# Performance work log

Hardware: AMD Instinct MI355X
Metric: run time of the kernel (lower is better)

The kernel has to match this reference:

```python
import jax, jax.numpy as jnp
import numpy as np

B, LQ, LKV, D, H, LOOKBACK = 4, 4096, 512, 512, 8, 8
DH = D // H
SCALE = DH ** -0.5


def setup_inputs() -> dict:
    key = jax.random.key(0)
    ks = jax.random.split(key, 12)
    q = jax.random.normal(ks[0], (B, LQ, D), dtype=jnp.float32)
    kv_src = jax.random.normal(ks[1], (B, LKV, D), dtype=jnp.float32)
    seg_id = jnp.sort(jax.random.randint(ks[2], (B, LQ), 0, LKV), axis=-1)
    kv_mask = jnp.zeros((B, LKV), dtype=bool)
    q_pad_mask = jnp.zeros((B, LQ), dtype=bool)
    s = D ** -0.5
    Wq = jax.random.normal(ks[3], (D, D), jnp.float32) * s
    bq = jnp.zeros((D,), jnp.float32)
    Wk = jax.random.normal(ks[4], (D, D), jnp.float32) * s
    bk = jnp.zeros((D,), jnp.float32)
    Wv = jax.random.normal(ks[5], (D, D), jnp.float32) * s
    bv = jnp.zeros((D,), jnp.float32)
    Wo = jax.random.normal(ks[6], (D, D), jnp.float32) * s
    bo = jnp.zeros((D,), jnp.float32)
    return {"q": q, "kv_src": kv_src, "seg_id": seg_id, "kv_mask": kv_mask,
            "q_pad_mask": q_pad_mask, "Wq": Wq, "bq": bq, "Wk": Wk, "bk": bk,
            "Wv": Wv, "bv": bv, "Wo": Wo, "bo": bo}


def _split_heads(x):
    b, l, _ = x.shape
    return x.reshape(b, l, H, DH).transpose(0, 2, 1, 3)  # (B,H,L,Dh)


def reference(q, kv_src, seg_id, kv_mask, q_pad_mask, Wq, bq, Wk, bk, Wv, bv, Wo, bo):
    qh = _split_heads(q @ Wq + bq)        # (B,H,Lq,Dh)
    kh = _split_heads(kv_src @ Wk + bk)   # (B,H,Lkv,Dh)
    vh = _split_heads(kv_src @ Wv + bv)   # (B,H,Lkv,Dh)

    offsets = jnp.arange(LOOKBACK + 1)
    gather = jnp.clip(seg_id[:, :, None] - offsets, 0, LKV - 1)  # (B,Lq,Kw)

    # per-batch windowed gather of K/V: (B,H,Lq,Kw,Dh)
    k_sel = jax.vmap(lambda kb, gb: kb[:, gb])(kh, gather)
    v_sel = jax.vmap(lambda vb, gb: vb[:, gb])(vh, gather)

    scores = jnp.einsum('bhld,bhlkd->bhlk', qh, k_sel) * SCALE
    mask_sel = jax.vmap(lambda m, g: m[g])(kv_mask, gather)  # (B,Lq,Kw)
    scores = jnp.where(mask_sel[:, None], jnp.finfo(scores.dtype).min, scores)
    probs = jax.nn.softmax(scores, axis=-1)

    out = jnp.einsum('bhlk,bhlkd->bhld', probs, v_sel)
    out = out.transpose(0, 2, 1, 3).reshape(q.shape[0], q.shape[1], D)
    out = out @ Wo + bo
    out = jnp.where(q_pad_mask[:, :, None], 0.0, out)
    return out
```

## Files before the change

kernel.cpp:

```cpp
#include <hip/hip_runtime.h>
#include <hip/hip_bf16.h>
#include <float.h>

typedef unsigned short u16;
typedef __attribute__((ext_vector_type(8))) short short8;
typedef __attribute__((ext_vector_type(4))) float f32x4;

#define NB       4
#define LQ       4096
#define LKV      512
#define DMODEL   512
#define NH       8
#define DH       64
#define KW       9
#define SCALE    0.125f

#define BM 64
#define BN 128
#define BK 32

__device__ inline float bf2f(u16 v) { return __uint_as_float(((unsigned)v) << 16); }
__device__ inline u16 f2bf(float f) {
    unsigned u = __float_as_uint(f);
    return (u16)((u + 0x7fffu + ((u >> 16) & 1u)) >> 16);
}
__device__ inline void gload16(const u16* g, u16* l) {
    __builtin_amdgcn_global_load_lds((const __attribute__((address_space(1))) void*)g,
                                     (__attribute__((address_space(3))) void*)l, 16, 0, 0);
}
__device__ inline short8 cvt8(const float4 v0, const float4 v1) {
    short8 s;
    s[0] = (short)f2bf(v0.x); s[1] = (short)f2bf(v0.y);
    s[2] = (short)f2bf(v0.z); s[3] = (short)f2bf(v0.w);
    s[4] = (short)f2bf(v1.x); s[5] = (short)f2bf(v1.y);
    s[6] = (short)f2bf(v1.z); s[7] = (short)f2bf(v1.w);
    return s;
}
__device__ inline int xcd_swz(int id, int nwg) {
    const int cpx = nwg >> 3;
    return (id & 7) * cpx + (id >> 3);
}

__global__ __launch_bounds__(256) void transpose4_kernel(
    const float* __restrict__ Wq, const float* __restrict__ Wk,
    const float* __restrict__ Wv, const float* __restrict__ Wo,
    u16* __restrict__ Wqt, u16* __restrict__ Wkvt, u16* __restrict__ Wot)
{
    __shared__ float tile[32][33];
    const int z = blockIdx.z;
    const float* src = (z == 0) ? Wq : (z == 1) ? Wk : (z == 2) ? Wv : Wo;
    u16* dst = (z == 0) ? Wqt : (z == 3) ? Wot : Wkvt;
    const int roff = (z == 2) ? DMODEL : 0;

    const int tx = threadIdx.x & 31, ty = threadIdx.x >> 5;
    const int x0 = blockIdx.x * 32, y0 = blockIdx.y * 32;
    #pragma unroll
    for (int i = 0; i < 4; ++i)
        tile[ty + i * 8][tx] = src[(y0 + ty + i * 8) * DMODEL + x0 + tx];
    __syncthreads();
    #pragma unroll
    for (int i = 0; i < 4; ++i)
        dst[(long long)(roff + x0 + ty + i * 8) * DMODEL + y0 + tx] = f2bf(tile[tx][ty + i * 8]);
}

template<int A_F32, int OUT_F32>
__global__ __launch_bounds__(256, 6) void gemm64_kernel(
    const void* __restrict__ Ain, const u16* __restrict__ Bt,
    const float* __restrict__ bias0, const float* __restrict__ bias1, int nsplit,
    void* __restrict__ Cout, int M, int N, int K, int cshift,
    const unsigned char* __restrict__ row_mask)
{
    __shared__ u16 As[BM * BK];
    __shared__ u16 Bs[BN * BK];

    const int tid = threadIdx.x;
    const int w = tid >> 6, l = tid & 63;
    const int wr = w >> 1, wc = w & 1;

    const int wg = xcd_swz((int)blockIdx.x, (int)gridDim.x);
    const int bx = wg & ((1 << cshift) - 1);
    const int by = wg >> cshift;
    const int brow = by * BM, bcol = bx * BN;

    const int rsub = l >> 2;
    const int csrc = (l & 3) ^ (rsub & 3);
    const u16*   gA  = (const u16*)Ain   + (long long)(brow + w * 16 + rsub) * K + csrc * 8;
    const float* gAf = (const float*)Ain + (long long)(brow + w * 16 + rsub) * K + csrc * 8;
    const u16* gB0 = Bt + (long long)(bcol + w * 32 + rsub) * K + csrc * 8;
    const u16* gB1 = gB0 + (long long)16 * K;
    u16* lA  = As + (w * 16) * BK;
    u16* lB0 = Bs + (w * 32) * BK;
    u16* lB1 = Bs + (w * 32 + 16) * BK;

    const int hi = l >> 4, lr = l & 15;
    const int cs = ((hi ^ (lr & 3)) * 8);

    f32x4 acc[2][4] = {};

    float4 v0, v1;
    if (A_F32) { v0 = *(const float4*)(gAf); v1 = *(const float4*)(gAf + 4); }

    for (int k0 = 0; k0 < K; k0 += BK) {
        if (A_F32) {
            *(short8*)(lA + l * 8) = cvt8(v0, v1);
        } else {
            gload16(gA + k0, lA);
        }
        gload16(gB0 + k0, lB0);
        gload16(gB1 + k0, lB1);
        __syncthreads();

        if (A_F32 && k0 + BK < K) {
            v0 = *(const float4*)(gAf + k0 + BK);
            v1 = *(const float4*)(gAf + k0 + BK + 4);
        }

        short8 a[2], b[4];
        #pragma unroll
        for (int m = 0; m < 2; ++m)
            a[m] = *(const short8*)&As[(wr * 32 + m * 16 + lr) * BK + cs];
        #pragma unroll
        for (int n = 0; n < 4; ++n)
            b[n] = *(const short8*)&Bs[(wc * 64 + n * 16 + lr) * BK + cs];
        #pragma unroll
        for (int m = 0; m < 2; ++m)
            #pragma unroll
            for (int n = 0; n < 4; ++n)
                acc[m][n] = __builtin_amdgcn_mfma_f32_16x16x32_bf16(a[m], b[n], acc[m][n], 0, 0, 0);
        __syncthreads();
    }

    #pragma unroll
    for (int m = 0; m < 2; ++m) {
        #pragma unroll
        for (int n = 0; n < 4; ++n) {
            const int col = bcol + wc * 64 + n * 16 + lr;
            const float bv = (col < nsplit) ? bias0[col] : bias1[col - nsplit];
            #pragma unroll
            for (int r = 0; r < 4; ++r) {
                const int row = brow + wr * 32 + m * 16 + hi * 4 + r;
                const float v = acc[m][n][r] + bv;
                if (OUT_F32) {
                    ((float*)Cout)[(long long)row * N + col] =
                        (row_mask != nullptr && row_mask[row]) ? 0.0f : v;
                } else {
                    ((u16*)Cout)[(long long)row * N + col] = f2bf(v);
                }
            }
        }
    }
}

__global__ __launch_bounds__(256, 6) void qproj_attn_kernel(
    const float* __restrict__ Aq, const u16* __restrict__ Bt,
    const float* __restrict__ bias, const u16* __restrict__ khv,
    const int* __restrict__ seg_id, const unsigned char* __restrict__ kv_mask,
    u16* __restrict__ atb)
{
    __shared__ u16 smem[BM * BN];
    u16* As = smem;
    u16* Bs = smem + BM * BK;
    u16* qt = smem;

    const int tid = threadIdx.x;
    const int w = tid >> 6, l = tid & 63;
    const int wr = w >> 1, wc = w & 1;

    const int wg = xcd_swz((int)blockIdx.x, (int)gridDim.x);
    const int bx = wg & 3;
    const int by = wg >> 2;
    const int brow = by * BM, bcol = bx * BN;
    const int K = DMODEL;

    const int rsub = l >> 2;
    const int csrc = (l & 3) ^ (rsub & 3);
    const float* gAf = Aq + (long long)(brow + w * 16 + rsub) * K + csrc * 8;
    const u16* gB0 = Bt + (long long)(bcol + w * 32 + rsub) * K + csrc * 8;
    const u16* gB1 = gB0 + (long long)16 * K;
    u16* lA  = As + (w * 16) * BK;
    u16* lB0 = Bs + (w * 32) * BK;
    u16* lB1 = Bs + (w * 32 + 16) * BK;

    const int hi = l >> 4, lr = l & 15;
    const int cs = ((hi ^ (lr & 3)) * 8);

    f32x4 acc[2][4] = {};

    float4 v0 = *(const float4*)(gAf);
    float4 v1 = *(const float4*)(gAf + 4);

    for (int k0 = 0; k0 < K; k0 += BK) {
        *(short8*)(lA + l * 8) = cvt8(v0, v1);
        gload16(gB0 + k0, lB0);
        gload16(gB1 + k0, lB1);
        __syncthreads();

        if (k0 + BK < K) {
            v0 = *(const float4*)(gAf + k0 + BK);
            v1 = *(const float4*)(gAf + k0 + BK + 4);
        }

        short8 a[2], b[4];
        #pragma unroll
        for (int m = 0; m < 2; ++m)
            a[m] = *(const short8*)&As[(wr * 32 + m * 16 + lr) * BK + cs];
        #pragma unroll
        for (int n = 0; n < 4; ++n)
            b[n] = *(const short8*)&Bs[(wc * 64 + n * 16 + lr) * BK + cs];
        #pragma unroll
        for (int m = 0; m < 2; ++m)
            #pragma unroll
            for (int n = 0; n < 4; ++n)
                acc[m][n] = __builtin_amdgcn_mfma_f32_16x16x32_bf16(a[m], b[n], acc[m][n], 0, 0, 0);
        __syncthreads();
    }

    #pragma unroll
    for (int m = 0; m < 2; ++m) {
        #pragma unroll
        for (int n = 0; n < 4; ++n) {
            const int col = wc * 64 + n * 16 + lr;
            const float bv = bias[bcol + col];
            const int g = col >> 3;
            #pragma unroll
            for (int r = 0; r < 4; ++r) {
                const int row = wr * 32 + m * 16 + hi * 4 + r;
                qt[row * BN + ((g ^ (row & 7)) << 3) + (col & 7)] =
                    f2bf(acc[m][n][r] + bv);
            }
        }
    }
    __syncthreads();

    const int dchunk = tid & 7;
    #pragma unroll
    for (int p = 0; p < 4; ++p) {
        const int it = p * 32 + (tid >> 3);
        const int row = it >> 1;
        const int h2  = it & 1;
        const long long bl = brow + row;
        const int b = (int)(bl >> 12);
        const int head = (bcol >> 6) + h2;
        const int seg = seg_id[bl];
        const unsigned char* km = kv_mask + b * LKV;
        const u16* kvb = khv + (long long)b * LKV * 1024;

        const int g = h2 * 8 + dchunk;
        const short8 q8 = *(const short8*)&qt[row * BN + ((g ^ (row & 7)) << 3)];
        float qf[8];
        #pragma unroll
        for (int e = 0; e < 8; ++e) qf[e] = bf2f((u16)q8[e]);

        int idxs[KW];
        float sc[KW];
        #pragma unroll
        for (int j = 0; j < KW; ++j) {
            int idx = seg - j;
            idx = idx < 0 ? 0 : (idx > LKV - 1 ? LKV - 1 : idx);
            idxs[j] = idx;
            const short8 k8 = *(const short8*)&kvb[(long long)idx * 1024 + head * DH + dchunk * 8];
            float d = 0.0f;
            #pragma unroll
            for (int e = 0; e < 8; ++e)
                d = fmaf(qf[e], bf2f((u16)k8[e]), d);
            d += __shfl_xor(d, 1);
            d += __shfl_xor(d, 2);
            d += __shfl_xor(d, 4);
            float s = d * SCALE;
            if (km[idx]) s = -FLT_MAX;
            sc[j] = s;
        }

        float mx = sc[0];
        #pragma unroll
        for (int j = 1; j < KW; ++j) mx = fmaxf(mx, sc[j]);
        float den = 0.0f;
        #pragma unroll
        for (int j = 0; j < KW; ++j) { sc[j] = __expf(sc[j] - mx); den += sc[j]; }
        const float inv = 1.0f / den;

        float o[8];
        #pragma unroll
        for (int e = 0; e < 8; ++e) o[e] = 0.0f;
        #pragma unroll
        for (int j = 0; j < KW; ++j) {
            const short8 v8 = *(const short8*)&kvb[(long long)idxs[j] * 1024 + DMODEL + head * DH + dchunk * 8];
            const float pj = sc[j];
            #pragma unroll
            for (int e = 0; e < 8; ++e)
                o[e] = fmaf(pj, bf2f((u16)v8[e]), o[e]);
        }

        short8 ov;
        #pragma unroll
        for (int e = 0; e < 8; ++e) ov[e] = (short)f2bf(o[e] * inv);
        *(short8*)&atb[bl * DMODEL + head * DH + dchunk * 8] = ov;
    }
}

extern "C" void kernel_launch(void* const* d_in, const int* in_sizes, int n_in,
                              void* d_out, int out_size, void* d_ws, size_t ws_size,
                              hipStream_t stream) {
    const float*         q          = (const float*)d_in[0];
    const float*         kv_src     = (const float*)d_in[1];
    const int*           seg_id     = (const int*)d_in[2];
    const unsigned char* kv_mask    = (const unsigned char*)d_in[3];
    const unsigned char* q_pad_mask = (const unsigned char*)d_in[4];
    const float*         Wq         = (const float*)d_in[5];
    const float*         bq         = (const float*)d_in[6];
    const float*         Wk         = (const float*)d_in[7];
    const float*         bk         = (const float*)d_in[8];
    const float*         Wv         = (const float*)d_in[9];
    const float*         bv         = (const float*)d_in[10];
    const float*         Wo         = (const float*)d_in[11];
    const float*         bo         = (const float*)d_in[12];
    float* out = (float*)d_out;

    const long long MQ  = (long long)NB * LQ;
    const long long MKV = (long long)NB * LKV;

    char* wsb = (char*)d_ws;
    u16* Wqt  = (u16*)wsb;  wsb += DMODEL * DMODEL * 2;
    u16* Wkvt = (u16*)wsb;  wsb += 2 * DMODEL * DMODEL * 2;
    u16* Wot  = (u16*)wsb;  wsb += DMODEL * DMODEL * 2;
    u16* khv  = (u16*)wsb;  wsb += MKV * 2 * DMODEL * 2;
    u16* atb  = (u16*)wsb;  wsb += MQ  * DMODEL * 2;

    dim3 blk(256);

    transpose4_kernel<<<dim3(DMODEL / 32, DMODEL / 32, 4), blk, 0, stream>>>(
        Wq, Wk, Wv, Wo, Wqt, Wkvt, Wot);

    gemm64_kernel<1, 0><<<dim3((unsigned)((2 * DMODEL / BN) * (MKV / BM))), blk, 0, stream>>>(
        kv_src, Wkvt, bk, bv, DMODEL, khv, (int)MKV, 2 * DMODEL, DMODEL, 3, nullptr);

    qproj_attn_kernel<<<dim3((unsigned)((DMODEL / BN) * (MQ / BM))), blk, 0, stream>>>(
        q, Wqt, bq, khv, seg_id, kv_mask, atb);

    gemm64_kernel<0, 1><<<dim3((unsigned)((DMODEL / BN) * (MQ / BM))), blk, 0, stream>>>(
        atb, Wot, bo, bo, DMODEL, out, (int)MQ, DMODEL, DMODEL, 2, q_pad_mask);
}
```

Measured before the change: 83.09 us.

## Retile GEMMs to 64x64x64 with one head per attention block

Changes the GEMM tile from 64x128 (BK 32) to 64x64 (BK 64), with an 8-chunk XOR swizzle for LDS and two MFMA k-steps per tile. It raises launch-bounds occupancy from 6 to 8 and doubles the grid. In the fused Q-projection/attention kernel each block now covers one head, so the attention phase handles 64 rows with 2 iterations instead of 4. The intent is more parallelism and fewer barrier rounds per K step, at the cost of less B-tile reuse per block and more redundant A-tile loads.

```diff
diff --git a/kernel.cpp b/kernel.cpp
--- a/kernel.cpp
+++ b/kernel.cpp
@@ -16,8 +16,8 @@
 #define SCALE    0.125f
 
 #define BM 64
-#define BN 128
-#define BK 32
+#define BN 64
+#define BK 64
 
 __device__ inline float bf2f(u16 v) { return __uint_as_float(((unsigned)v) << 16); }
 __device__ inline u16 f2bf(float f) {
@@ -64,10 +64,10 @@
 }
 
 template<int A_F32, int OUT_F32>
-__global__ __launch_bounds__(256, 6) void gemm64_kernel(
+__global__ __launch_bounds__(256, 8) void gemm64_kernel(
     const void* __restrict__ Ain, const u16* __restrict__ Bt,
     const float* __restrict__ bias0, const float* __restrict__ bias1, int nsplit,
-    void* __restrict__ Cout, int M, int N, int K, int cshift,
+    void* __restrict__ Cout, int N, int K, int cshift,
     const unsigned char* __restrict__ row_mask)
 {
     __shared__ u16 As[BM * BK];
@@ -82,59 +82,73 @@
     const int by = wg >> cshift;
     const int brow = by * BM, bcol = bx * BN;
 
-    const int rsub = l >> 2;
-    const int csrc = (l & 3) ^ (rsub & 3);
-    const u16*   gA  = (const u16*)Ain   + (long long)(brow + w * 16 + rsub) * K + csrc * 8;
-    const float* gAf = (const float*)Ain + (long long)(brow + w * 16 + rsub) * K + csrc * 8;
-    const u16* gB0 = Bt + (long long)(bcol + w * 32 + rsub) * K + csrc * 8;
-    const u16* gB1 = gB0 + (long long)16 * K;
-    u16* lA  = As + (w * 16) * BK;
-    u16* lB0 = Bs + (w * 32) * BK;
-    u16* lB1 = Bs + (w * 32 + 16) * BK;
+    const int srow   = l >> 3;
+    const int schunk = ((l & 7) ^ srow) * 8;
+    const long long ar0 = brow + w * 16 + srow;
+    const long long br0 = bcol + w * 16 + srow;
+    const u16*   gA0  = (const u16*)Ain   + ar0 * K + schunk;
+    const u16*   gA1  = gA0 + 8 * K;
+    const float* gAf0 = (const float*)Ain + ar0 * K + schunk;
+    const float* gAf1 = gAf0 + 8 * K;
+    const u16* gB0 = Bt + br0 * K + schunk;
+    const u16* gB1 = gB0 + 8 * K;
+    u16* lA0 = As + (w * 16) * BK;
+    u16* lA1 = As + (w * 16 + 8) * BK;
+    u16* lB0 = Bs + (w * 16) * BK;
+    u16* lB1 = Bs + (w * 16 + 8) * BK;
 
     const int hi = l >> 4, lr = l & 15;
-    const int cs = ((hi ^ (lr & 3)) * 8);
-
-    f32x4 acc[2][4] = {};
-
-    float4 v0, v1;
-    if (A_F32) { v0 = *(const float4*)(gAf); v1 = *(const float4*)(gAf + 4); }
+    const int r7 = lr & 7;
+
+    f32x4 acc[2][2] = {};
+
+    float4 p0, p1, p2, p3;
+    if (A_F32) {
+        p0 = *(const float4*)(gAf0);     p1 = *(const float4*)(gAf0 + 4);
+        p2 = *(const float4*)(gAf1);     p3 = *(const float4*)(gAf1 + 4);
+    }
 
     for (int k0 = 0; k0 < K; k0 += BK) {
         if (A_F32) {
-            *(short8*)(lA + l * 8) = cvt8(v0, v1);
+            *(short8*)(lA0 + l * 8) = cvt8(p0, p1);
+            *(short8*)(lA1 + l * 8) = cvt8(p2, p3);
         } else {
-            gload16(gA + k0, lA);
+            gload16(gA0 + k0, lA0);
+            gload16(gA1 + k0, lA1);
         }
         gload16(gB0 + k0, lB0);
         gload16(gB1 + k0, lB1);
         __syncthreads();
 
         if (A_F32 && k0 + BK < K) {
-            v0 = *(const float4*)(gAf + k0 + BK);
-            v1 = *(const float4*)(gAf + k0 + BK + 4);
-        }
-
-        short8 a[2], b[4];
-        #pragma unroll
-        for (int m = 0; m < 2; ++m)
-            a[m] = *(const short8*)&As[(wr * 32 + m * 16 + lr) * BK + cs];
-        #pragma unroll
-        for (int n = 0; n < 4; ++n)
-            b[n] = *(const short8*)&Bs[(wc * 64 + n * 16 + lr) * BK + cs];
-        #pragma unroll
-        for (int m = 0; m < 2; ++m)
-            #pragma unroll
-            for (int n = 0; n < 4; ++n)
-                acc[m][n] = __builtin_amdgcn_mfma_f32_16x16x32_bf16(a[m], b[n], acc[m][n], 0, 0, 0);
+            p0 = *(const float4*)(gAf0 + k0 + BK); p1 = *(const float4*)(gAf0 + k0 + BK + 4);
+            p2 = *(const float4*)(gAf1 + k0 + BK); p3 = *(const float4*)(gAf1 + k0 + BK + 4);
+        }
+
+        #pragma unroll
+        for (int g2 = 0; g2 < 2; ++g2) {
+            const int slot = ((g2 * 4 + hi) ^ r7) * 8;
+            short8 a[2], b[2];
+            #pragma unroll
+            for (int m = 0; m < 2; ++m)
+                a[m] = *(const short8*)&As[(wr * 32 + m * 16 + lr) * BK + slot];
+            #pragma unroll
+            for (int n = 0; n < 2; ++n)
+                b[n] = *(const short8*)&Bs[(wc * 32 + n * 16 + lr) * BK + slot];
+            #pragma unroll
+            for (int m = 0; m < 2; ++m)
+                #pragma unroll
+                for (int n = 0; n < 2; ++n)
+                    acc[m][n] = __builtin_amdgcn_mfma_f32_16x16x32_bf16(a[m], b[n], acc[m][n], 0, 0, 0);
+        }
         __syncthreads();
     }
 
     #pragma unroll
     for (int m = 0; m < 2; ++m) {
         #pragma unroll
-        for (int n = 0; n < 4; ++n) {
-            const int col = bcol + wc * 64 + n * 16 + lr;
+        for (int n = 0; n < 2; ++n) {
+            const int col = bcol + wc * 32 + n * 16 + lr;
             const float bv = (col < nsplit) ? bias0[col] : bias1[col - nsplit];
             #pragma unroll
             for (int r = 0; r < 4; ++r) {
@@ -151,13 +165,13 @@
     }
 }
 
-__global__ __launch_bounds__(256, 6) void qproj_attn_kernel(
+__global__ __launch_bounds__(256, 8) void qproj_attn_kernel(
     const float* __restrict__ Aq, const u16* __restrict__ Bt,
     const float* __restrict__ bias, const u16* __restrict__ khv,
     const int* __restrict__ seg_id, const unsigned char* __restrict__ kv_mask,
     u16* __restrict__ atb)
 {
-    __shared__ u16 smem[BM * BN];
+    __shared__ u16 smem[BM * BK + BN * BK];
     u16* As = smem;
     u16* Bs = smem + BM * BK;
     u16* qt = smem;
@@ -167,65 +181,73 @@
     const int wr = w >> 1, wc = w & 1;
 
     const int wg = xcd_swz((int)blockIdx.x, (int)gridDim.x);
-    const int bx = wg & 3;
-    const int by = wg >> 2;
+    const int bx = wg & 7;
+    const int by = wg >> 3;
     const int brow = by * BM, bcol = bx * BN;
     const int K = DMODEL;
 
-    const int rsub = l >> 2;
-    const int csrc = (l & 3) ^ (rsub & 3);
-    const float* gAf = Aq + (long long)(brow + w * 16 + rsub) * K + csrc * 8;
-    const u16* gB0 = Bt + (long long)(bcol + w * 32 + rsub) * K + csrc * 8;
-    const u16* gB1 = gB0 + (long long)16 * K;
-    u16* lA  = As + (w * 16) * BK;
-    u16* lB0 = Bs + (w * 32) * BK;
-    u16* lB1 = Bs + (w * 32 + 16) * BK;
+    const int srow   = l >> 3;
+    const int schunk = ((l & 7) ^ srow) * 8;
+    const long long ar0 = brow + w * 16 + srow;
+    const long long br0 = bcol + w * 16 + srow;
+    const float* gAf0 = Aq + ar0 * K + schunk;
+    const float* gAf1 = gAf0 + 8 * K;
+    const u16* gB0 = Bt + br0 * K + schunk;
+    const u16* gB1 = gB0 + 8 * K;
+    u16* lA0 = As + (w * 16) * BK;
+    u16* lA1 = As + (w * 16 + 8) * BK;
+    u16* lB0 = Bs + (w * 16) * BK;
+    u16* lB1 = Bs + (w * 16 + 8) * BK;
 
     const int hi = l >> 4, lr = l & 15;
-    const int cs = ((hi ^ (lr & 3)) * 8);
-
-    f32x4 acc[2][4] = {};
-
-    float4 v0 = *(const float4*)(gAf);
-    float4 v1 = *(const float4*)(gAf + 4);
+    const int r7 = lr & 7;
+
+    f32x4 acc[2][2] = {};
+
+    float4 p0 = *(const float4*)(gAf0), p1 = *(const float4*)(gAf0 + 4);
+    float4 p2 = *(const float4*)(gAf1), p3 = *(const float4*)(gAf1 + 4);
 
     for (int k0 = 0; k0 < K; k0 += BK) {
-        *(short8*)(lA + l * 8) = cvt8(v0, v1);
+        *(short8*)(lA0 + l * 8) = cvt8(p0, p1);
+        *(short8*)(lA1 + l * 8) = cvt8(p2, p3);
         gload16(gB0 + k0, lB0);
         gload16(gB1 + k0, lB1);
         __syncthreads();
 
         if (k0 + BK < K) {
-            v0 = *(const float4*)(gAf + k0 + BK);
-            v1 = *(const float4*)(gAf + k0 + BK + 4);
-        }
-
-        short8 a[2], b[4];
-        #pragma unroll
-        for (int m = 0; m < 2; ++m)
-            a[m] = *(const short8*)&As[(wr * 32 + m * 16 + lr) * BK + cs];
-        #pragma unroll
-        for (int n = 0; n < 4; ++n)
-            b[n] = *(const short8*)&Bs[(wc * 64 + n * 16 + lr) * BK + cs];
-        #pragma unroll
-        for (int m = 0; m < 2; ++m)
-            #pragma unroll
-            for (int n = 0; n < 4; ++n)
-                acc[m][n] = __builtin_amdgcn_mfma_f32_16x16x32_bf16(a[m], b[n], acc[m][n], 0, 0, 0);
+            p0 = *(const float4*)(gAf0 + k0 + BK); p1 = *(const float4*)(gAf0 + k0 + BK + 4);
+            p2 = *(const float4*)(gAf1 + k0 + BK); p3 = *(const float4*)(gAf1 + k0 + BK + 4);
+        }
+
+        #pragma unroll
+        for (int g2 = 0; g2 < 2; ++g2) {
+            const int slot = ((g2 * 4 + hi) ^ r7) * 8;
+            short8 a[2], b[2];
+            #pragma unroll
+            for (int m = 0; m < 2; ++m)
+                a[m] = *(const short8*)&As[(wr * 32 + m * 16 + lr) * BK + slot];
+            #pragma unroll
+            for (int n = 0; n < 2; ++n)
+                b[n] = *(const short8*)&Bs[(wc * 32 + n * 16 + lr) * BK + slot];
+            #pragma unroll
+            for (int m = 0; m < 2; ++m)
+                #pragma unroll
+                for (int n = 0; n < 2; ++n)
+                    acc[m][n] = __builtin_amdgcn_mfma_f32_16x16x32_bf16(a[m], b[n], acc[m][n], 0, 0, 0);
+        }
         __syncthreads();
     }
 
     #pragma unroll
     for (int m = 0; m < 2; ++m) {
         #pragma unroll
-        for (int n = 0; n < 4; ++n) {
-            const int col = wc * 64 + n * 16 + lr;
+        for (int n = 0; n < 2; ++n) {
+            const int col = wc * 32 + n * 16 + lr;
             const float bv = bias[bcol + col];
-            const int g = col >> 3;
             #pragma unroll
             for (int r = 0; r < 4; ++r) {
                 const int row = wr * 32 + m * 16 + hi * 4 + r;
-                qt[row * BN + ((g ^ (row & 7)) << 3) + (col & 7)] =
+                qt[row * BN + (((col >> 3) ^ (row & 7)) << 3) + (col & 7)] =
                     f2bf(acc[m][n][r] + bv);
             }
         }
@@ -233,20 +255,17 @@
     __syncthreads();
 
     const int dchunk = tid & 7;
-    #pragma unroll
-    for (int p = 0; p < 4; ++p) {
-        const int it = p * 32 + (tid >> 3);
-        const int row = it >> 1;
-        const int h2  = it & 1;
+    const int head = bx;
+    #pragma unroll
+    for (int p = 0; p < 2; ++p) {
+        const int row = p * 32 + (tid >> 3);
         const long long bl = brow + row;
         const int b = (int)(bl >> 12);
-        const int head = (bcol >> 6) + h2;
         const int seg = seg_id[bl];
         const unsigned char* km = kv_mask + b * LKV;
         const u16* kvb = khv + (long long)b * LKV * 1024;
 
-        const int g = h2 * 8 + dchunk;
-        const short8 q8 = *(const short8*)&qt[row * BN + ((g ^ (row & 7)) << 3)];
+        const short8 q8 = *(const short8*)&qt[row * BN + ((dchunk ^ (row & 7)) << 3)];
         float qf[8];
         #pragma unroll
         for (int e = 0; e < 8; ++e) qf[e] = bf2f((u16)q8[e]);
@@ -332,11 +351,11 @@
         Wq, Wk, Wv, Wo, Wqt, Wkvt, Wot);
 
     gemm64_kernel<1, 0><<<dim3((unsigned)((2 * DMODEL / BN) * (MKV / BM))), blk, 0, stream>>>(
-        kv_src, Wkvt, bk, bv, DMODEL, khv, (int)MKV, 2 * DMODEL, DMODEL, 3, nullptr);
+        kv_src, Wkvt, bk, bv, DMODEL, khv, 2 * DMODEL, DMODEL, 4, nullptr);
 
     qproj_attn_kernel<<<dim3((unsigned)((DMODEL / BN) * (MQ / BM))), blk, 0, stream>>>(
         q, Wqt, bq, khv, seg_id, kv_mask, atb);
 
     gemm64_kernel<0, 1><<<dim3((unsigned)((DMODEL / BN) * (MQ / BM))), blk, 0, stream>>>(
-        atb, Wot, bo, bo, DMODEL, out, (int)MQ, DMODEL, DMODEL, 2, q_pad_mask);
-}
+        atb, Wot, bo, bo, DMODEL, out, DMODEL, DMODEL, 3, q_pad_mask);
+}
```

Result: faster. 72.98 us (-12.2%).
